# Kernel tuning notes

Measured on AMD Instinct MI355X. Metric: run time of the kernel, lower is better.

The kernel has to match this reference:

```python
import jax, jax.numpy as jnp
import numpy as np

B, C, H = 16, 256, 32          # batch, in_channels(=out_channels), image_size
HEADS, HS = 8, 32              # heads = out_channels // head_size
D = HEADS * HS                 # head_dim = 256
N = H * H                      # tokens = 1024
EPS = 1e-5


def _rel_indices(h, w):
    # Faithful port of RelativeAttention2d.get_indices
    y = np.arange(h)
    x = np.arange(w)
    y1, x1, y2, x2 = np.meshgrid(y, x, y, x, indexing='ij')
    idx = (y1 - y2 + h - 1) * (2 * w - 1) + (x1 - x2 + w - 1)
    return jnp.asarray(idx.reshape(-1), dtype=jnp.int32)  # [N*N]


def setup_inputs() -> dict:
    key = jax.random.key(0)
    ks = jax.random.split(key, 10)
    s = 0.02
    return {
        'x': jax.random.normal(ks[0], (B, C, H, H), jnp.float32),
        'ln_g': jnp.ones((C,), jnp.float32),
        'ln_b': jnp.zeros((C,), jnp.float32),
        'wq': jax.random.normal(ks[1], (D, C), jnp.float32) * s,
        'bq': jnp.zeros((D,), jnp.float32),
        'wk': jax.random.normal(ks[2], (D, C), jnp.float32) * s,
        'bk': jnp.zeros((D,), jnp.float32),
        'wv': jax.random.normal(ks[3], (D, C), jnp.float32) * s,
        'bv': jnp.zeros((D,), jnp.float32),
        'wo': jax.random.normal(ks[4], (C, D), jnp.float32) * s,
        'bo': jnp.zeros((C,), jnp.float32),
        'rel_bias': jax.random.normal(ks[5], (HEADS, (2 * H - 1) * (2 * H - 1)), jnp.float32),
        'rel_idx': _rel_indices(H, H),
    }


def reference(x, ln_g, ln_b, wq, bq, wk, bk, wv, bv, wo, bo, rel_bias, rel_idx):
    b = x.shape[0]
    # norm(): LayerNorm over channel axis (dim 1 after the double transpose)
    mu = jnp.mean(x, axis=1, keepdims=True)
    var = jnp.mean((x - mu) ** 2, axis=1, keepdims=True)
    xn = (x - mu) / jnp.sqrt(var + EPS)
    xn = xn * ln_g[None, :, None, None] + ln_b[None, :, None, None]
    # reshape_for_linear: raw reshape [b, C, H, W] -> [b, N, C] (as in torch)
    xr = xn.reshape(b, N, C)
    # projections, then raw view(b, heads, head_size, -1) as in torch
    q = (xr @ wq.T + bq).reshape(b, HEADS, HS, N)
    k = (xr @ wk.T + bk).reshape(b, HEADS, HS, N)
    v = (xr @ wv.T + bv).reshape(b, HEADS, HS, N)
    # dots = k^T q / sqrt(head_dim)   [b, heads, N, N]
    dots = jnp.einsum('bhdn,bhdm->bhnm', k, q) / np.float32(np.sqrt(D))
    # gathered relative position bias  [heads, N, N]
    bias = rel_bias[:, rel_idx].reshape(HEADS, N, N)
    attn = jax.nn.softmax(dots + bias[None], axis=-2)  # non-standard softmax dim
    # out = v @ attn  [b, heads, head_size, N]
    out = jnp.einsum('bhdn,bhnm->bhdm', v, attn)
    out = out.reshape(b, H, H, D)  # raw view as in torch
    out = out @ wo.T + bo          # to_output linear (dropout is identity in eval)
    out = out.reshape(b, C, H, H)  # raw view back to [b, out_channels, H, W]
    return x + out
```

## Files before the change

### kernel.cpp

```cpp
#include <hip/hip_runtime.h>
#include <cstdint>

#define PERB 262144

typedef __attribute__((ext_vector_type(8))) short bf16x8;
typedef __attribute__((ext_vector_type(4))) float f32x4;
typedef unsigned short ushort_t;

__device__ __forceinline__ uint16_t f2bf(float f) {
    uint32_t u = __float_as_uint(f);
    u += 0x7fff + ((u >> 16) & 1);
    return (uint16_t)(u >> 16);
}

__device__ __forceinline__ void glds16(const void* g, void* l) {
    __builtin_amdgcn_global_load_lds(
        (const __attribute__((address_space(1))) void*)g,
        (__attribute__((address_space(3))) void*)l, 16, 0, 0);
}

__global__ __launch_bounds__(256) void prep_kernel(
    const float* __restrict__ x, const float* __restrict__ gam,
    const float* __restrict__ bet, ushort_t* __restrict__ X,
    const float* __restrict__ wq, const float* __restrict__ wk,
    const float* __restrict__ wv, const float* __restrict__ wo,
    ushort_t* __restrict__ oq, ushort_t* __restrict__ ok,
    ushort_t* __restrict__ ov, ushort_t* __restrict__ oo)
{
    const int blk = blockIdx.x;
    const int tid = threadIdx.x;
    if (blk < 256) {
        const int which = blk >> 6;
        const int idx = ((blk & 63) * 256 + tid) * 4;
        const float* src = which == 0 ? wq : which == 1 ? wk : which == 2 ? wv : wo;
        ushort_t* dst    = which == 0 ? oq : which == 1 ? ok : which == 2 ? ov : oo;
        const float4 v = *(const float4*)&src[idx];
        uint2 p;
        p.x = (uint32_t)f2bf(v.x) | ((uint32_t)f2bf(v.y) << 16);
        p.y = (uint32_t)f2bf(v.z) | ((uint32_t)f2bf(v.w) << 16);
        *(uint2*)&dst[idx] = p;
        return;
    }
    const int lb  = blk - 256;
    const int b   = lb >> 5;
    const int sp0 = (lb & 31) << 5;
    const int spl = tid & 31;
    const int cg  = tid >> 5;
    const int c0  = cg << 5;
    const int sp  = sp0 + spl;
    const float* xb = x + (size_t)b * PERB + sp;

    float vals[32];
    float s = 0.f, sq = 0.f;
#pragma unroll
    for (int i = 0; i < 32; ++i) {
        float v = xb[(size_t)(c0 + i) * 1024];
        vals[i] = v; s += v; sq += v * v;
    }
    __shared__ float rs[8][32];
    __shared__ float rq[8][32];
    rs[cg][spl] = s; rq[cg][spl] = sq;
    __syncthreads();
    float ts = 0.f, tq = 0.f;
#pragma unroll
    for (int g = 0; g < 8; ++g) { ts += rs[g][spl]; tq += rq[g][spl]; }
    const float mean = ts * (1.f / 256.f);
    const float var  = tq * (1.f / 256.f) - mean * mean;
    const float rstd = rsqrtf(var + 1e-5f);

    ushort_t* Xb = X + (size_t)b * PERB + sp;
#pragma unroll
    for (int i = 0; i < 32; ++i) {
        const int cc = c0 + i;
        Xb[(size_t)cc * 1024] = f2bf((vals[i] - mean) * rstd * gam[cc] + bet[cc]);
    }
}

__device__ __forceinline__ void qkv_stage(
    ushort_t* Sb, const ushort_t* __restrict__ X,
    const ushort_t* __restrict__ wq, const ushort_t* __restrict__ wk,
    const ushort_t* __restrict__ wv,
    int m0, int n0, int k0, int w, int lane)
{
    const int rsub = lane >> 3;
    const int u    = lane & 7;
    const int koct = u ^ rsub;
#pragma unroll
    for (int i = 0; i < 2; ++i) {
        const int rg  = w * 2 + i;
        const int row = rg * 8 + rsub;
        const int go  = k0 + koct * 8;
        ushort_t* db = Sb + rg * 512;
        glds16(&X [(size_t)(m0 + row) * 256 + go], db);
        glds16(&wq[(size_t)(n0 + row) * 256 + go], db + 4096);
        glds16(&wk[(size_t)(n0 + row) * 256 + go], db + 8192);
        glds16(&wv[(size_t)(n0 + row) * 256 + go], db + 12288);
    }
}

__device__ __forceinline__ void qkv_compute(
    const ushort_t* Sb, int w, int c, int quad, f32x4 acc[3][4])
{
#pragma unroll
    for (int ks = 0; ks < 2; ++ks) {
        const int kq = ks * 4 + quad;
        const int uo = (kq ^ (c & 7)) * 8;
        bf16x8 af[4];
#pragma unroll
        for (int msub = 0; msub < 4; ++msub)
            af[msub] = *(const bf16x8*)&Sb[(msub * 16 + c) * 64 + uo];
        bf16x8 bw[3];
#pragma unroll
        for (int o3 = 0; o3 < 3; ++o3)
            bw[o3] = *(const bf16x8*)&Sb[(o3 + 1) * 4096 + (w * 16 + c) * 64 + uo];
#pragma unroll
        for (int o3 = 0; o3 < 3; ++o3)
#pragma unroll
            for (int msub = 0; msub < 4; ++msub)
                acc[o3][msub] = __builtin_amdgcn_mfma_f32_16x16x32_bf16(
                    bw[o3], af[msub], acc[o3][msub], 0, 0, 0);
    }
}

__global__ __launch_bounds__(256) void qkv_kernel(
    const ushort_t* __restrict__ X,
    const ushort_t* __restrict__ wq, const float* __restrict__ bq,
    const ushort_t* __restrict__ wk, const float* __restrict__ bk,
    const ushort_t* __restrict__ wv, const float* __restrict__ bv,
    ushort_t* __restrict__ Q, ushort_t* __restrict__ K, ushort_t* __restrict__ V)
{
    __shared__ __align__(16) ushort_t SB0[4][4096];
    __shared__ __align__(16) ushort_t SB1[4][4096];

    const int blk = blockIdx.x;
    const int m0  = (blk >> 2) << 6;
    const int n0  = (blk & 3) << 6;
    const int tid = threadIdx.x;
    const int w    = tid >> 6;
    const int lane = tid & 63;
    const int quad = lane >> 4;
    const int c    = lane & 15;

    f32x4 acc[3][4];
#pragma unroll
    for (int o3 = 0; o3 < 3; ++o3)
#pragma unroll
        for (int i = 0; i < 4; ++i) acc[o3][i] = (f32x4){0.f, 0.f, 0.f, 0.f};

    qkv_stage(&SB0[0][0], X, wq, wk, wv, m0, n0, 0, w, lane);
    __syncthreads();
#pragma unroll
    for (int kc = 0; kc < 4; ++kc) {
        if (kc < 3) {
            if ((kc & 1) == 0)
                qkv_stage(&SB1[0][0], X, wq, wk, wv, m0, n0, (kc + 1) << 6, w, lane);
            else
                qkv_stage(&SB0[0][0], X, wq, wk, wv, m0, n0, (kc + 1) << 6, w, lane);
        }
        if ((kc & 1) == 0) qkv_compute(&SB0[0][0], w, c, quad, acc);
        else               qkv_compute(&SB1[0][0], w, c, quad, acc);
        __syncthreads();
    }

    const int n = n0 + w * 16 + quad * 4;
    const float4 bq4 = *(const float4*)&bq[n];
    const float4 bk4 = *(const float4*)&bk[n];
    const float4 bv4 = *(const float4*)&bv[n];
    ushort_t* outs[3] = {Q, K, V};
    const float4 bias[3] = {bq4, bk4, bv4};
#pragma unroll
    for (int msub = 0; msub < 4; ++msub) {
        const size_t m = (size_t)(m0 + msub * 16 + c);
#pragma unroll
        for (int o3 = 0; o3 < 3; ++o3) {
            const f32x4 a = acc[o3][msub];
            uint2 p;
            p.x = (uint32_t)f2bf(a[0] + bias[o3].x) | ((uint32_t)f2bf(a[1] + bias[o3].y) << 16);
            p.y = (uint32_t)f2bf(a[2] + bias[o3].z) | ((uint32_t)f2bf(a[3] + bias[o3].w) << 16);
            *(uint2*)&outs[o3][m * 256 + n] = p;
        }
    }
}

#define C1F 0.09016844005556022f
#define LOG2EF 1.4426950408889634f

__global__ __launch_bounds__(256, 4) void attn_kernel(
    const ushort_t* __restrict__ Q, const ushort_t* __restrict__ K,
    const ushort_t* __restrict__ V, const float* __restrict__ relb,
    ushort_t* __restrict__ O)
{
    __shared__ __align__(16) unsigned char smem[28672];
    char* Pb = (char*)smem;
    char* Kl = (char*)(smem + 16384);
    char* Vl = (char*)(smem + 20480);

    const int blk = blockIdx.x;
    const int bh  = blk & 127;
    const int mt  = blk >> 7;
    const int b   = bh >> 3;
    const int h   = bh & 7;
    const int m0  = mt << 7;
    const int tid = threadIdx.x;
    const int w    = tid >> 6;
    const int lane = tid & 63;
    const int quad = lane >> 4;
    const int c    = lane & 15;

    const size_t base = (size_t)b * PERB + (size_t)h * 32768;
    const ushort_t* Qg = Q + base;
    const ushort_t* Kg = K + base;
    const ushort_t* Vg = V + base;
    const float* rbh = relb + h * 3969;

    {
        const int mm = tid & 127;
        const int sg = tid >> 7;
        union { bf16x8 v; uint16_t u[8]; } g0, g1;
#pragma unroll
        for (int j = 0; j < 8; ++j)
            g0.u[j] = Qg[(size_t)(sg * 16 + j) * 1024 + m0 + mm];
#pragma unroll
        for (int j = 0; j < 8; ++j)
            g1.u[j] = Qg[(size_t)(sg * 16 + 8 + j) * 1024 + m0 + mm];
        *(bf16x8*)(Pb + (sg * 2 + 0) * 2048 + mm * 16) = g0.v;
        *(bf16x8*)(Pb + (sg * 2 + 1) * 2048 + mm * 16) = g1.v;
    }
    __syncthreads();
    bf16x8 qfrag[8];
#pragma unroll
    for (int msub = 0; msub < 8; ++msub)
        qfrag[msub] = *(const bf16x8*)(Pb + quad * 2048 + (msub * 16 + c) * 16);

    int moff[8];
#pragma unroll
    for (int msub = 0; msub < 8; ++msub) {
        const int m = m0 + msub * 16 + c;
        moff[msub] = 1984 - (m >> 5) * 63 - (m & 31);
    }

    f32x4 oacc[2][2], dacc[2];
#pragma unroll
    for (int i = 0; i < 2; ++i) {
        dacc[i] = (f32x4){0.f, 0.f, 0.f, 0.f};
#pragma unroll
        for (int j = 0; j < 2; ++j) oacc[i][j] = (f32x4){0.f, 0.f, 0.f, 0.f};
    }
    bf16x8 onesf;
#pragma unroll
    for (int j = 0; j < 8; ++j) onesf[j] = (short)0x3F80;

    const int knn = tid & 63, ksg = tid >> 6;
    const int vs  = tid >> 3, vng = tid & 7;
    const int kWr = ksg * 1024 + knn * 16;
    const int vWr = vs * 128 + ((vng ^ (vs & 7)) << 4);
    const int kRd = quad * 1024 + (w * 16 + c) * 16;
    const int pWr = c * 128 + (((2 * w + (quad >> 1)) ^ (c & 7)) << 4) + ((quad & 1) << 3);
    const int c7  = c & 7;

    uint32_t kpre[8]; bf16x8 vpre;
#pragma unroll
    for (int j = 0; j < 8; ++j) kpre[j] = Kg[(size_t)(ksg * 8 + j) * 1024 + knn];
    vpre = *(const bf16x8*)&Vg[(size_t)vs * 1024 + vng * 8];

    for (int ch = 0; ch < 16; ++ch) {
        const int n0c = ch << 6;
        const int cb  = ch & 1;

        {
            uint4 kp;
            kp.x = kpre[0] | (kpre[1] << 16);
            kp.y = kpre[2] | (kpre[3] << 16);
            kp.z = kpre[4] | (kpre[5] << 16);
            kp.w = kpre[6] | (kpre[7] << 16);
            *(uint4*)(Kl + kWr) = kp;
            *(bf16x8*)(Vl + cb * 4096 + vWr) = vpre;
        }
        __syncthreads();

        {
            const int n0n = ((ch + 1) & 15) << 6;
#pragma unroll
            for (int j = 0; j < 8; ++j)
                kpre[j] = Kg[(size_t)(ksg * 8 + j) * 1024 + n0n + knn];
            vpre = *(const bf16x8*)&Vg[(size_t)vs * 1024 + n0n + vng * 8];
        }

        const bf16x8 kf = *(const bf16x8*)(Kl + kRd);
        f32x4 sacc[8];
#pragma unroll
        for (int msub = 0; msub < 8; ++msub) {
            const f32x4 z = {0.f, 0.f, 0.f, 0.f};
            sacc[msub] = __builtin_amdgcn_mfma_f32_16x16x32_bf16(kf, qfrag[msub], z, 0, 0, 0);
        }

        const int nbase = n0c + w * 16 + quad * 4;
        const int nidx0 = (nbase >> 5) * 63 + (nbase & 31);
#pragma unroll
        for (int msub = 0; msub < 8; ++msub) {
            const float* bp = rbh + nidx0 + moff[msub];
            float p[4];
#pragma unroll
            for (int r = 0; r < 4; ++r)
                p[r] = __builtin_amdgcn_exp2f(fmaf(bp[r], LOG2EF, sacc[msub][r] * C1F));
            uint2 pk;
            pk.x = __builtin_amdgcn_perm(__float_as_uint(p[1]), __float_as_uint(p[0]), 0x07060302u);
            pk.y = __builtin_amdgcn_perm(__float_as_uint(p[3]), __float_as_uint(p[2]), 0x07060302u);
            *(uint2*)(Pb + msub * 2048 + pWr) = pk;
        }
        __syncthreads();

#pragma unroll
        for (int kstep = 0; kstep < 2; ++kstep) {
            const int u = ((kstep * 4 + quad) ^ c7) << 4;
            const bf16x8 vf0 = *(const bf16x8*)(Vl + cb * 4096 + c * 128 + u);
            const bf16x8 vf1 = *(const bf16x8*)(Vl + cb * 4096 + (16 + c) * 128 + u);
#pragma unroll
            for (int mi = 0; mi < 2; ++mi) {
                const bf16x8 pf = *(const bf16x8*)(Pb + ((w * 2 + mi) * 16 + c) * 128 + u);
                oacc[0][mi] = __builtin_amdgcn_mfma_f32_16x16x32_bf16(vf0, pf, oacc[0][mi], 0, 0, 0);
                oacc[1][mi] = __builtin_amdgcn_mfma_f32_16x16x32_bf16(vf1, pf, oacc[1][mi], 0, 0, 0);
                dacc[mi]    = __builtin_amdgcn_mfma_f32_16x16x32_bf16(onesf, pf, dacc[mi], 0, 0, 0);
            }
        }
    }

    ushort_t* Ob = O + base;
#pragma unroll
    for (int mi = 0; mi < 2; ++mi) {
        const float inv = 1.0f / dacc[mi][0];
        const int m = m0 + (w * 2 + mi) * 16 + c;
#pragma unroll
        for (int ssub = 0; ssub < 2; ++ssub)
#pragma unroll
            for (int r = 0; r < 4; ++r)
                Ob[(size_t)(ssub * 16 + quad * 4 + r) * 1024 + m] = f2bf(oacc[ssub][mi][r] * inv);
    }
}

__device__ __forceinline__ void oproj_stage(
    ushort_t* Sb, const ushort_t* __restrict__ A, const ushort_t* __restrict__ wo,
    int m0, int n0, int k0, int w, int lane)
{
    const int rsub = lane >> 3;
    const int u    = lane & 7;
    const int koct = u ^ rsub;
#pragma unroll
    for (int i = 0; i < 2; ++i) {
        const int rg  = w * 2 + i;
        const int row = rg * 8 + rsub;
        const int go  = k0 + koct * 8;
        ushort_t* db = Sb + rg * 512;
        glds16(&A [(size_t)(m0 + row) * 256 + go], db);
        glds16(&wo[(size_t)(n0 + row) * 256 + go], db + 4096);
    }
}

__device__ __forceinline__ void oproj_compute(
    const ushort_t* Sb, int w, int c, int quad, f32x4 acc[4])
{
#pragma unroll
    for (int ks = 0; ks < 2; ++ks) {
        const int kq = ks * 4 + quad;
        const int uo = (kq ^ (c & 7)) * 8;
        const bf16x8 bw = *(const bf16x8*)&Sb[4096 + (w * 16 + c) * 64 + uo];
#pragma unroll
        for (int msub = 0; msub < 4; ++msub) {
            const bf16x8 af = *(const bf16x8*)&Sb[(msub * 16 + c) * 64 + uo];
            acc[msub] = __builtin_amdgcn_mfma_f32_16x16x32_bf16(bw, af, acc[msub], 0, 0, 0);
        }
    }
}

__global__ __launch_bounds__(256, 4) void oproj_kernel(
    const ushort_t* __restrict__ A, const ushort_t* __restrict__ wo,
    const float* __restrict__ bo, const float* __restrict__ x,
    float* __restrict__ out)
{
    __shared__ __align__(16) ushort_t SA0[2][4096];
    __shared__ __align__(16) ushort_t SA1[2][4096];

    const int blk = blockIdx.x;
    const int m0  = (blk >> 2) << 6;
    const int n0  = (blk & 3) << 6;
    const int tid = threadIdx.x;
    const int w    = tid >> 6;
    const int lane = tid & 63;
    const int quad = lane >> 4;
    const int c    = lane & 15;

    f32x4 acc[4];
#pragma unroll
    for (int i = 0; i < 4; ++i) acc[i] = (f32x4){0.f, 0.f, 0.f, 0.f};

    oproj_stage(&SA0[0][0], A, wo, m0, n0, 0, w, lane);
    __syncthreads();
#pragma unroll
    for (int kc = 0; kc < 4; ++kc) {
        if (kc < 3) {
            if ((kc & 1) == 0)
                oproj_stage(&SA1[0][0], A, wo, m0, n0, (kc + 1) << 6, w, lane);
            else
                oproj_stage(&SA0[0][0], A, wo, m0, n0, (kc + 1) << 6, w, lane);
        }
        if ((kc & 1) == 0) oproj_compute(&SA0[0][0], w, c, quad, acc);
        else               oproj_compute(&SA1[0][0], w, c, quad, acc);
        __syncthreads();
    }

    const int n = n0 + w * 16 + quad * 4;
    const float4 bo4 = *(const float4*)&bo[n];
#pragma unroll
    for (int msub = 0; msub < 4; ++msub) {
        const size_t g = (size_t)(m0 + msub * 16 + c) * 256 + n;
        const float4 r = *(const float4*)&x[g];
        float4 t;
        t.x = acc[msub][0] + bo4.x + r.x;
        t.y = acc[msub][1] + bo4.y + r.y;
        t.z = acc[msub][2] + bo4.z + r.z;
        t.w = acc[msub][3] + bo4.w + r.w;
        *(float4*)&out[g] = t;
    }
}

extern "C" void kernel_launch(void* const* d_in, const int* in_sizes, int n_in,
                              void* d_out, int out_size, void* d_ws, size_t ws_size,
                              hipStream_t stream)
{
    (void)in_sizes; (void)n_in; (void)out_size; (void)ws_size;
    const float* x   = (const float*)d_in[0];
    const float* lng = (const float*)d_in[1];
    const float* lnb = (const float*)d_in[2];
    const float* wq  = (const float*)d_in[3];
    const float* bq  = (const float*)d_in[4];
    const float* wk  = (const float*)d_in[5];
    const float* bk  = (const float*)d_in[6];
    const float* wv  = (const float*)d_in[7];
    const float* bv  = (const float*)d_in[8];
    const float* wo  = (const float*)d_in[9];
    const float* bo  = (const float*)d_in[10];
    const float* rb  = (const float*)d_in[11];

    ushort_t* ws = (ushort_t*)d_ws;
    ushort_t* Xbf = ws;
    ushort_t* Qbf = ws + 1 * 4194304;
    ushort_t* Kbf = ws + 2 * 4194304;
    ushort_t* Vbf = ws + 3 * 4194304;
    ushort_t* Obf = ws + 4 * 4194304;
    ushort_t* Wqb = ws + 5 * 4194304;
    ushort_t* Wkb = Wqb + 65536;
    ushort_t* Wvb = Wkb + 65536;
    ushort_t* Wob = Wvb + 65536;
    float* out = (float*)d_out;

    hipLaunchKernelGGL(prep_kernel,  dim3(768),  dim3(256), 0, stream,
                       x, lng, lnb, Xbf, wq, wk, wv, wo, Wqb, Wkb, Wvb, Wob);
    hipLaunchKernelGGL(qkv_kernel,   dim3(1024), dim3(256), 0, stream,
                       Xbf, Wqb, bq, Wkb, bk, Wvb, bv, Qbf, Kbf, Vbf);
    hipLaunchKernelGGL(attn_kernel,  dim3(1024), dim3(256), 0, stream, Qbf, Kbf, Vbf, rb, Obf);
    hipLaunchKernelGGL(oproj_kernel, dim3(1024), dim3(256), 0, stream, Obf, Wob, bo, x, out);
}
```

Before: 161.2 us.

## Store Q/K transposed per head and stream K/V into LDS with async loads

The QKV projection now writes Q and K in a per-head transposed layout (token-major, 32 contiguous head elements), so the attention kernel reads them with wide contiguous loads instead of strided 2-byte gathers. K and V tiles are double-buffered in LDS and filled with global_load_lds direct-to-LDS copies issued one chunk ahead, which removes the register staging and repacking. s_setprio hints are placed around the MFMA sections. This costs more LDS (32 KB per block, which may affect occupancy) and relies on the async LDS loads having finished by the next barrier.

Result: slower. 168.8 us (+4.7%).

```diff
diff --git a/kernel.cpp b/kernel.cpp
--- a/kernel.cpp
+++ b/kernel.cpp
@@ -127,7 +127,7 @@
     const ushort_t* __restrict__ wq, const float* __restrict__ bq,
     const ushort_t* __restrict__ wk, const float* __restrict__ bk,
     const ushort_t* __restrict__ wv, const float* __restrict__ bv,
-    ushort_t* __restrict__ Q, ushort_t* __restrict__ K, ushort_t* __restrict__ V)
+    ushort_t* __restrict__ QT, ushort_t* __restrict__ KT, ushort_t* __restrict__ V)
 {
     __shared__ __align__(16) ushort_t SB0[4][4096];
     __shared__ __align__(16) ushort_t SB1[4][4096];
@@ -166,19 +166,28 @@
     const float4 bq4 = *(const float4*)&bq[n];
     const float4 bk4 = *(const float4*)&bk[n];
     const float4 bv4 = *(const float4*)&bv[n];
-    ushort_t* outs[3] = {Q, K, V};
-    const float4 bias[3] = {bq4, bk4, bv4};
+    const int h_ = n >> 5;
+    const int s_ = n & 31;
 #pragma unroll
     for (int msub = 0; msub < 4; ++msub) {
-        const size_t m = (size_t)(m0 + msub * 16 + c);
-#pragma unroll
-        for (int o3 = 0; o3 < 3; ++o3) {
-            const f32x4 a = acc[o3][msub];
-            uint2 p;
-            p.x = (uint32_t)f2bf(a[0] + bias[o3].x) | ((uint32_t)f2bf(a[1] + bias[o3].y) << 16);
-            p.y = (uint32_t)f2bf(a[2] + bias[o3].z) | ((uint32_t)f2bf(a[3] + bias[o3].w) << 16);
-            *(uint2*)&outs[o3][m * 256 + n] = p;
-        }
+        const int m = m0 + msub * 16 + c;
+        const f32x4 av = acc[2][msub];
+        uint2 pv;
+        pv.x = (uint32_t)f2bf(av[0] + bv4.x) | ((uint32_t)f2bf(av[1] + bv4.y) << 16);
+        pv.y = (uint32_t)f2bf(av[2] + bv4.z) | ((uint32_t)f2bf(av[3] + bv4.w) << 16);
+        *(uint2*)&V[(size_t)m * 256 + n] = pv;
+        const size_t tb = (size_t)(m >> 10) * PERB + (size_t)h_ * 32768
+                        + (size_t)(m & 1023) * 32 + s_;
+        const f32x4 aq = acc[0][msub];
+        uint2 pq;
+        pq.x = (uint32_t)f2bf(aq[0] + bq4.x) | ((uint32_t)f2bf(aq[1] + bq4.y) << 16);
+        pq.y = (uint32_t)f2bf(aq[2] + bq4.z) | ((uint32_t)f2bf(aq[3] + bq4.w) << 16);
+        *(uint2*)&QT[tb] = pq;
+        const f32x4 ak = acc[1][msub];
+        uint2 pk;
+        pk.x = (uint32_t)f2bf(ak[0] + bk4.x) | ((uint32_t)f2bf(ak[1] + bk4.y) << 16);
+        pk.y = (uint32_t)f2bf(ak[2] + bk4.z) | ((uint32_t)f2bf(ak[3] + bk4.w) << 16);
+        *(uint2*)&KT[tb] = pk;
     }
 }
 
@@ -186,14 +195,14 @@
 #define LOG2EF 1.4426950408889634f
 
 __global__ __launch_bounds__(256, 4) void attn_kernel(
-    const ushort_t* __restrict__ Q, const ushort_t* __restrict__ K,
+    const ushort_t* __restrict__ QT, const ushort_t* __restrict__ KT,
     const ushort_t* __restrict__ V, const float* __restrict__ relb,
     ushort_t* __restrict__ O)
 {
-    __shared__ __align__(16) unsigned char smem[28672];
+    __shared__ __align__(16) unsigned char smem[32768];
     char* Pb = (char*)smem;
     char* Kl = (char*)(smem + 16384);
-    char* Vl = (char*)(smem + 20480);
+    char* Vl = (char*)(smem + 24576);
 
     const int blk = blockIdx.x;
     const int bh  = blk & 127;
@@ -208,23 +217,27 @@
     const int c    = lane & 15;
 
     const size_t base = (size_t)b * PERB + (size_t)h * 32768;
-    const ushort_t* Qg = Q + base;
-    const ushort_t* Kg = K + base;
-    const ushort_t* Vg = V + base;
+    const ushort_t* QTg = QT + base;
+    const ushort_t* KTg = KT + base;
+    const ushort_t* Vg  = V + base;
     const float* rbh = relb + h * 3969;
+
+    const ushort_t* kSrc = &KTg[(size_t)lane * 32 + w * 8];
+    const int vd = tid >> 3, vu = tid & 7;
+    const ushort_t* vSrc = &Vg[(size_t)vd * 1024 + ((vu ^ (vd & 7)) << 3)];
+    char* kDst = Kl + w * 1024;
+    char* vDst = Vl + w * 1024;
+    glds16(kSrc, kDst);
+    glds16(vSrc, vDst);
+    kSrc += 2048;  vSrc += 64;
 
     {
         const int mm = tid & 127;
-        const int sg = tid >> 7;
-        union { bf16x8 v; uint16_t u[8]; } g0, g1;
-#pragma unroll
-        for (int j = 0; j < 8; ++j)
-            g0.u[j] = Qg[(size_t)(sg * 16 + j) * 1024 + m0 + mm];
-#pragma unroll
-        for (int j = 0; j < 8; ++j)
-            g1.u[j] = Qg[(size_t)(sg * 16 + 8 + j) * 1024 + m0 + mm];
-        *(bf16x8*)(Pb + (sg * 2 + 0) * 2048 + mm * 16) = g0.v;
-        *(bf16x8*)(Pb + (sg * 2 + 1) * 2048 + mm * 16) = g1.v;
+        const int sg2 = tid >> 7;
+        const bf16x8 q0 = *(const bf16x8*)&QTg[(size_t)(m0 + mm) * 32 + sg2 * 16];
+        const bf16x8 q1 = *(const bf16x8*)&QTg[(size_t)(m0 + mm) * 32 + sg2 * 16 + 8];
+        *(bf16x8*)(Pb + (sg2 * 2 + 0) * 2048 + mm * 16) = q0;
+        *(bf16x8*)(Pb + (sg2 * 2 + 1) * 2048 + mm * 16) = q1;
     }
     __syncthreads();
     bf16x8 qfrag[8];
@@ -250,51 +263,32 @@
 #pragma unroll
     for (int j = 0; j < 8; ++j) onesf[j] = (short)0x3F80;
 
-    const int knn = tid & 63, ksg = tid >> 6;
-    const int vs  = tid >> 3, vng = tid & 7;
-    const int kWr = ksg * 1024 + knn * 16;
-    const int vWr = vs * 128 + ((vng ^ (vs & 7)) << 4);
     const int kRd = quad * 1024 + (w * 16 + c) * 16;
     const int pWr = c * 128 + (((2 * w + (quad >> 1)) ^ (c & 7)) << 4) + ((quad & 1) << 3);
     const int c7  = c & 7;
 
-    uint32_t kpre[8]; bf16x8 vpre;
-#pragma unroll
-    for (int j = 0; j < 8; ++j) kpre[j] = Kg[(size_t)(ksg * 8 + j) * 1024 + knn];
-    vpre = *(const bf16x8*)&Vg[(size_t)vs * 1024 + vng * 8];
-
     for (int ch = 0; ch < 16; ++ch) {
-        const int n0c = ch << 6;
-        const int cb  = ch & 1;
-
-        {
-            uint4 kp;
-            kp.x = kpre[0] | (kpre[1] << 16);
-            kp.y = kpre[2] | (kpre[3] << 16);
-            kp.z = kpre[4] | (kpre[5] << 16);
-            kp.w = kpre[6] | (kpre[7] << 16);
-            *(uint4*)(Kl + kWr) = kp;
-            *(bf16x8*)(Vl + cb * 4096 + vWr) = vpre;
-        }
+        const int cb = ch & 1;
         __syncthreads();
 
-        {
-            const int n0n = ((ch + 1) & 15) << 6;
-#pragma unroll
-            for (int j = 0; j < 8; ++j)
-                kpre[j] = Kg[(size_t)(ksg * 8 + j) * 1024 + n0n + knn];
-            vpre = *(const bf16x8*)&Vg[(size_t)vs * 1024 + n0n + vng * 8];
-        }
-
-        const bf16x8 kf = *(const bf16x8*)(Kl + kRd);
+        if (ch < 15) {
+            const int nb = (cb ^ 1) << 12;
+            glds16(kSrc, kDst + nb);
+            glds16(vSrc, vDst + nb);
+            kSrc += 2048;  vSrc += 64;
+        }
+
+        const bf16x8 kf = *(const bf16x8*)(Kl + (cb << 12) + kRd);
         f32x4 sacc[8];
+        __builtin_amdgcn_s_setprio(1);
 #pragma unroll
         for (int msub = 0; msub < 8; ++msub) {
             const f32x4 z = {0.f, 0.f, 0.f, 0.f};
             sacc[msub] = __builtin_amdgcn_mfma_f32_16x16x32_bf16(kf, qfrag[msub], z, 0, 0, 0);
         }
-
-        const int nbase = n0c + w * 16 + quad * 4;
+        __builtin_amdgcn_s_setprio(0);
+
+        const int nbase = (ch << 6) + w * 16 + quad * 4;
         const int nidx0 = (nbase >> 5) * 63 + (nbase & 31);
 #pragma unroll
         for (int msub = 0; msub < 8; ++msub) {
@@ -310,11 +304,13 @@
         }
         __syncthreads();
 
+        const char* Vc = Vl + (cb << 12);
+        __builtin_amdgcn_s_setprio(1);
 #pragma unroll
         for (int kstep = 0; kstep < 2; ++kstep) {
             const int u = ((kstep * 4 + quad) ^ c7) << 4;
-            const bf16x8 vf0 = *(const bf16x8*)(Vl + cb * 4096 + c * 128 + u);
-            const bf16x8 vf1 = *(const bf16x8*)(Vl + cb * 4096 + (16 + c) * 128 + u);
+            const bf16x8 vf0 = *(const bf16x8*)(Vc + c * 128 + u);
+            const bf16x8 vf1 = *(const bf16x8*)(Vc + (16 + c) * 128 + u);
 #pragma unroll
             for (int mi = 0; mi < 2; ++mi) {
                 const bf16x8 pf = *(const bf16x8*)(Pb + ((w * 2 + mi) * 16 + c) * 128 + u);
@@ -323,6 +319,7 @@
                 dacc[mi]    = __builtin_amdgcn_mfma_f32_16x16x32_bf16(onesf, pf, dacc[mi], 0, 0, 0);
             }
         }
+        __builtin_amdgcn_s_setprio(0);
     }
 
     ushort_t* Ob = O + base;
```

## Prescale relative bias by log2e in prep and vectorize layernorm loads

Applied to the files above, without the earlier changes.

The prep kernel gains 8 blocks that write a copy of the relative-position bias multiplied by log2(e), so the attention inner loop drops one multiply per score and uses a single fma feeding exp2. The layernorm part of prep is restructured so each thread handles 4 contiguous spatial positions with float4 loads and packed bf16 stores. Each block now covers 64 spatial positions, which halves the layernorm block count, and a two-stage shared-memory reduction over 16 channel groups replaces the old 8-group one. This adds a small extra global buffer and one more synchronization in the layernorm path.

Result: no change. 161.7 us (+0.3%).

```diff
diff --git a/kernel.cpp b/kernel.cpp
--- a/kernel.cpp
+++ b/kernel.cpp
@@ -2,6 +2,8 @@
 #include <cstdint>
 
 #define PERB 262144
+#define LOG2EF 1.4426950408889634f
+#define C1F 0.09016844005556022f
 
 typedef __attribute__((ext_vector_type(8))) short bf16x8;
 typedef __attribute__((ext_vector_type(4))) float f32x4;
@@ -25,7 +27,8 @@
     const float* __restrict__ wq, const float* __restrict__ wk,
     const float* __restrict__ wv, const float* __restrict__ wo,
     ushort_t* __restrict__ oq, ushort_t* __restrict__ ok,
-    ushort_t* __restrict__ ov, ushort_t* __restrict__ oo)
+    ushort_t* __restrict__ ov, ushort_t* __restrict__ oo,
+    const float* __restrict__ rb, float* __restrict__ rb2)
 {
     const int blk = blockIdx.x;
     const int tid = threadIdx.x;
@@ -41,38 +44,62 @@
         *(uint2*)&dst[idx] = p;
         return;
     }
+    if (blk >= 512) {
+        const int h = blk - 512;
+        const float* s = rb + h * 3969;
+        float* d = rb2 + h * 3969;
+        for (int i = tid; i < 3969; i += 256) d[i] = s[i] * LOG2EF;
+        return;
+    }
     const int lb  = blk - 256;
-    const int b   = lb >> 5;
-    const int sp0 = (lb & 31) << 5;
-    const int spl = tid & 31;
-    const int cg  = tid >> 5;
-    const int c0  = cg << 5;
-    const int sp  = sp0 + spl;
+    const int b   = lb >> 4;
+    const int sp0 = (lb & 15) << 6;
+    const int v   = tid & 15;
+    const int cg  = tid >> 4;
+    const int sp  = sp0 + v * 4;
     const float* xb = x + (size_t)b * PERB + sp;
 
-    float vals[32];
-    float s = 0.f, sq = 0.f;
-#pragma unroll
-    for (int i = 0; i < 32; ++i) {
-        float v = xb[(size_t)(c0 + i) * 1024];
-        vals[i] = v; s += v; sq += v * v;
-    }
-    __shared__ float rs[8][32];
-    __shared__ float rq[8][32];
-    rs[cg][spl] = s; rq[cg][spl] = sq;
+    float4 vals[16];
+    float4 s4 = {0.f, 0.f, 0.f, 0.f}, q4 = {0.f, 0.f, 0.f, 0.f};
+#pragma unroll
+    for (int i = 0; i < 16; ++i) {
+        const float4 t = *(const float4*)&xb[(size_t)(cg * 16 + i) * 1024];
+        vals[i] = t;
+        s4.x += t.x; s4.y += t.y; s4.z += t.z; s4.w += t.w;
+        q4.x += t.x * t.x; q4.y += t.y * t.y; q4.z += t.z * t.z; q4.w += t.w * t.w;
+    }
+    __shared__ float red[2][16][64];
+    __shared__ float mr[2][64];
+    *(float4*)&red[0][cg][v * 4] = s4;
+    *(float4*)&red[1][cg][v * 4] = q4;
     __syncthreads();
-    float ts = 0.f, tq = 0.f;
-#pragma unroll
-    for (int g = 0; g < 8; ++g) { ts += rs[g][spl]; tq += rq[g][spl]; }
-    const float mean = ts * (1.f / 256.f);
-    const float var  = tq * (1.f / 256.f) - mean * mean;
-    const float rstd = rsqrtf(var + 1e-5f);
+    if (tid < 64) {
+        float ts = 0.f, tq = 0.f;
+#pragma unroll
+        for (int g = 0; g < 16; ++g) { ts += red[0][g][tid]; tq += red[1][g][tid]; }
+        const float mean = ts * (1.f / 256.f);
+        const float var  = tq * (1.f / 256.f) - mean * mean;
+        mr[0][tid] = mean;
+        mr[1][tid] = rsqrtf(var + 1e-5f);
+    }
+    __syncthreads();
+    const float4 mean4 = *(const float4*)&mr[0][v * 4];
+    const float4 rstd4 = *(const float4*)&mr[1][v * 4];
 
     ushort_t* Xb = X + (size_t)b * PERB + sp;
 #pragma unroll
-    for (int i = 0; i < 32; ++i) {
-        const int cc = c0 + i;
-        Xb[(size_t)cc * 1024] = f2bf((vals[i] - mean) * rstd * gam[cc] + bet[cc]);
+    for (int i = 0; i < 16; ++i) {
+        const int c = cg * 16 + i;
+        const float g = gam[c], be = bet[c];
+        const float4 t = vals[i];
+        const float y0 = (t.x - mean4.x) * rstd4.x * g + be;
+        const float y1 = (t.y - mean4.y) * rstd4.y * g + be;
+        const float y2 = (t.z - mean4.z) * rstd4.z * g + be;
+        const float y3 = (t.w - mean4.w) * rstd4.w * g + be;
+        uint2 p;
+        p.x = (uint32_t)f2bf(y0) | ((uint32_t)f2bf(y1) << 16);
+        p.y = (uint32_t)f2bf(y2) | ((uint32_t)f2bf(y3) << 16);
+        *(uint2*)&Xb[(size_t)c * 1024] = p;
     }
 }
 
@@ -182,12 +209,9 @@
     }
 }
 
-#define C1F 0.09016844005556022f
-#define LOG2EF 1.4426950408889634f
-
 __global__ __launch_bounds__(256, 4) void attn_kernel(
     const ushort_t* __restrict__ Q, const ushort_t* __restrict__ K,
-    const ushort_t* __restrict__ V, const float* __restrict__ relb,
+    const ushort_t* __restrict__ V, const float* __restrict__ relb2,
     ushort_t* __restrict__ O)
 {
     __shared__ __align__(16) unsigned char smem[28672];
@@ -211,7 +235,7 @@
     const ushort_t* Qg = Q + base;
     const ushort_t* Kg = K + base;
     const ushort_t* Vg = V + base;
-    const float* rbh = relb + h * 3969;
+    const float* rbh = relb2 + h * 3969;
 
     {
         const int mm = tid & 127;
@@ -302,7 +326,7 @@
             float p[4];
 #pragma unroll
             for (int r = 0; r < 4; ++r)
-                p[r] = __builtin_amdgcn_exp2f(fmaf(bp[r], LOG2EF, sacc[msub][r] * C1F));
+                p[r] = __builtin_amdgcn_exp2f(fmaf(sacc[msub][r], C1F, bp[r]));
             uint2 pk;
             pk.x = __builtin_amdgcn_perm(__float_as_uint(p[1]), __float_as_uint(p[0]), 0x07060302u);
             pk.y = __builtin_amdgcn_perm(__float_as_uint(p[3]), __float_as_uint(p[2]), 0x07060302u);
@@ -451,12 +475,13 @@
     ushort_t* Wkb = Wqb + 65536;
     ushort_t* Wvb = Wkb + 65536;
     ushort_t* Wob = Wvb + 65536;
+    float* rb2 = (float*)(Wob + 65536);
     float* out = (float*)d_out;
 
-    hipLaunchKernelGGL(prep_kernel,  dim3(768),  dim3(256), 0, stream,
-                       x, lng, lnb, Xbf, wq, wk, wv, wo, Wqb, Wkb, Wvb, Wob);
+    hipLaunchKernelGGL(prep_kernel,  dim3(520),  dim3(256), 0, stream,
+                       x, lng, lnb, Xbf, wq, wk, wv, wo, Wqb, Wkb, Wvb, Wob, rb, rb2);
     hipLaunchKernelGGL(qkv_kernel,   dim3(1024), dim3(256), 0, stream,
                        Xbf, Wqb, bq, Wkb, bk, Wvb, bv, Qbf, Kbf, Vbf);
-    hipLaunchKernelGGL(attn_kernel,  dim3(1024), dim3(256), 0, stream, Qbf, Kbf, Vbf, rb, Obf);
+    hipLaunchKernelGGL(attn_kernel,  dim3(1024), dim3(256), 0, stream, Qbf, Kbf, Vbf, rb2, Obf);
     hipLaunchKernelGGL(oproj_kernel, dim3(1024), dim3(256), 0, stream, Obf, Wob, bo, x, out);
 }
```
